# Optimization experiments

Measured on AMD Instinct MI355X. Metric: run time of the kernel, lower is better.

The kernel has to match this reference:

```python
import jax, jax.numpy as jnp
import numpy as np

N_NODES = 20000
N_EDGES = 160000
N_GRAPHS = 64
IN_DIM = 1304  # 1280 + 24
NEG_SLOPE = 0.2


def gat_conv(x, src, dst, W, a_src, a_dst, b, heads, out_ch):
    """PyG-style GATConv (source_to_target flow, self loops already appended).
    x: [N, in], W: [in, heads*out], a_src/a_dst: [heads, out], b: [heads*out].
    Returns [N, heads*out] (concat=True)."""
    N = x.shape[0]
    h = (x @ W).reshape(N, heads, out_ch)                 # [N, H, C]
    e_src = jnp.sum(h * a_src[None], axis=-1)             # [N, H]
    e_dst = jnp.sum(h * a_dst[None], axis=-1)             # [N, H]
    e = jax.nn.leaky_relu(e_src[src] + e_dst[dst], NEG_SLOPE)  # [E, H]
    # softmax over incoming edges of each destination node
    e_max = jax.ops.segment_max(e, dst, num_segments=N)   # [N, H]
    e_exp = jnp.exp(e - e_max[dst])
    denom = jax.ops.segment_sum(e_exp, dst, num_segments=N)
    alpha = e_exp / (denom[dst] + 1e-16)                  # [E, H]
    msg = h[src] * alpha[:, :, None]                      # [E, H, C]
    out = jax.ops.segment_sum(msg, dst, num_segments=N)   # [N, H, C]
    return out.reshape(N, heads * out_ch) + b


def setup_inputs() -> dict:
    key = jax.random.key(0)
    ks = jax.random.split(key, 20)
    x = jax.random.normal(ks[0], (N_NODES, IN_DIM), dtype=jnp.float32)
    edge_index = jax.random.randint(ks[1], (2, N_EDGES), 0, N_NODES, dtype=jnp.int32)
    phy = jax.random.normal(ks[2], (N_GRAPHS, 188), dtype=jnp.float32)
    batch = jnp.sort(jax.random.randint(ks[3], (N_NODES,), 0, N_GRAPHS, dtype=jnp.int32))

    def glorot(k, shape):
        fan_in, fan_out = shape[0], shape[-1]
        lim = jnp.sqrt(6.0 / (fan_in + fan_out))
        return jax.random.uniform(k, shape, jnp.float32, -lim, lim)

    params = {
        # conv1: GATConv(1304, 256, heads=3)
        "W1": glorot(ks[4], (IN_DIM, 3 * 256)),
        "a_src1": glorot(ks[5], (3, 256)) * 0.1,
        "a_dst1": glorot(ks[6], (3, 256)) * 0.1,
        "b1": jnp.zeros((3 * 256,), jnp.float32),
        # conv2: GATConv(768, 256, heads=1)
        "W2": glorot(ks[7], (3 * 256, 256)),
        "a_src2": glorot(ks[8], (1, 256)) * 0.1,
        "a_dst2": glorot(ks[9], (1, 256)) * 0.1,
        "b2": jnp.zeros((256,), jnp.float32),
        # fc1
        "fc1_w1": glorot(ks[10], (188, 128)), "fc1_b1": jnp.zeros((128,), jnp.float32),
        "fc1_w2": glorot(ks[11], (128, 128)), "fc1_b2": jnp.zeros((128,), jnp.float32),
        # fc2
        "fc2_w1": glorot(ks[12], (256 + 128, 192)), "fc2_b1": jnp.zeros((192,), jnp.float32),
        "fc2_w2": glorot(ks[13], (192, 2)), "fc2_b2": jnp.zeros((2,), jnp.float32),
    }
    return {"x": x, "edge_index": edge_index, "phy": phy, "batch": batch, **params}


def reference(x, edge_index, phy, batch,
              W1, a_src1, a_dst1, b1,
              W2, a_src2, a_dst2, b2,
              fc1_w1, fc1_b1, fc1_w2, fc1_b2,
              fc2_w1, fc2_b1, fc2_w2, fc2_b2):
    N = x.shape[0]
    # add self loops (PyG GATConv default)
    loops = jnp.arange(N, dtype=edge_index.dtype)
    src = jnp.concatenate([edge_index[0], loops])
    dst = jnp.concatenate([edge_index[1], loops])

    h = gat_conv(x, src, dst, W1, a_src1, a_dst1, b1, heads=3, out_ch=256)
    h = jax.nn.relu(h)  # dropout is identity at inference
    h = gat_conv(h, src, dst, W2, a_src2, a_dst2, b2, heads=1, out_ch=256)

    # global mean pool per graph
    sums = jax.ops.segment_sum(h, batch, num_segments=N_GRAPHS)        # [B, 256]
    cnts = jax.ops.segment_sum(jnp.ones((N,), h.dtype), batch, num_segments=N_GRAPHS)
    pooled = sums / jnp.maximum(cnts, 1.0)[:, None]

    mid = jax.nn.relu(phy @ fc1_w1 + fc1_b1)
    mid = jax.nn.relu(mid @ fc1_w2 + fc1_b2)

    z = jnp.concatenate([pooled, mid], axis=1)                          # [B, 384]
    z = jax.nn.relu(z @ fc2_w1 + fc2_b1)
    logits = z @ fc2_w2 + fc2_b2
    return jax.nn.softmax(logits, axis=1)
```

## Files before the change

### kernel.cpp

```cpp
#include <hip/hip_runtime.h>
#include <hip/hip_bf16.h>
#include <math.h>

#define NN    20000
#define MP1   20224
#define NP    20096
#define E0    160000
#define EL    180000
#define NG    64
#define INDIM 1304
#define K1P   1344
#define GNT   21
#define GNX   3
#define GMB   79
#define NEG_SLOPE 0.2f
#define PCH   8
#define NSB   20

#define ZB    80
#define XB    13272
#define WB    4800

typedef __bf16 bf16x8 __attribute__((ext_vector_type(8)));
typedef __bf16 bf16x4 __attribute__((ext_vector_type(4)));
typedef float  f32x4  __attribute__((ext_vector_type(4)));

__device__ __forceinline__ void gload16(const void* g, void* l) {
    __builtin_amdgcn_global_load_lds(
        (const __attribute__((address_space(1))) void*)g,
        (__attribute__((address_space(3))) void*)l, 16, 0, 0);
}

#define BAR()  { __builtin_amdgcn_s_barrier(); asm volatile("" ::: "memory"); }
#define VMW(n) { asm volatile("s_waitcnt vmcnt(" #n ")" ::: "memory"); __builtin_amdgcn_sched_barrier(0); }

__global__ __launch_bounds__(256)
void init_kernel(uint4* __restrict__ zreg, int n16,
                 const float* __restrict__ X, __hip_bfloat16* __restrict__ Xb,
                 const float* __restrict__ W1, const float* __restrict__ W2,
                 __hip_bfloat16* __restrict__ w1t, __hip_bfloat16* __restrict__ w2t) {
    const int b = blockIdx.x, t = threadIdx.x;
    if (b < ZB) {
        int i = b * 256 + t;
        if (i < n16) zreg[i] = (uint4){0u, 0u, 0u, 0u};
        return;
    }
    if (b < ZB + XB) {
        int idx = (b - ZB) * 256 + t;
        const int nb = K1P / 8;
        int row = idx / nb;
        int cb = (idx - row * nb) * 8;
        union { __hip_bfloat16 h[8]; float4 f4; } u;
        if (row < NN && cb + 8 <= INDIM) {
            const float4* p = (const float4*)(X + (size_t)row * INDIM + cb);
            float4 u0 = p[0], u1 = p[1];
            u.h[0] = __float2bfloat16(u0.x); u.h[1] = __float2bfloat16(u0.y);
            u.h[2] = __float2bfloat16(u0.z); u.h[3] = __float2bfloat16(u0.w);
            u.h[4] = __float2bfloat16(u1.x); u.h[5] = __float2bfloat16(u1.y);
            u.h[6] = __float2bfloat16(u1.z); u.h[7] = __float2bfloat16(u1.w);
        } else {
#pragma unroll
            for (int e = 0; e < 8; e++) {
                float f = (row < NN && cb + e < INDIM) ? X[(size_t)row * INDIM + cb + e] : 0.f;
                u.h[e] = __float2bfloat16(f);
            }
        }
        *(float4*)(Xb + (size_t)row * K1P + cb) = u.f4;
        return;
    }
    {
        int idx = (b - ZB - XB) * 256 + t;
        const int n1 = 768 * K1P;
        if (idx < n1) {
            int n = idx / K1P, k = idx - n * K1P;
            float f = (k < INDIM) ? W1[(size_t)k * 768 + n] : 0.f;
            w1t[idx] = __float2bfloat16(f);
        } else {
            int i2 = idx - n1;
            if (i2 < 256 * 768) {
                int n = i2 / 768, k = i2 - n * 768;
                w2t[i2] = __float2bfloat16(W2[(size_t)k * 256 + n]);
            }
        }
    }
}

__device__ __forceinline__ void stA(const __hip_bfloat16* __restrict__ A, int bm, int kt, int mh,
                                    char* abuf, int w, int l) {
#pragma unroll
    for (int u = 0; u < 2; u++) {
        int rl = (w << 3) + (l >> 3);
        int lrow = u * 128 + mh * 64 + rl;
        int skb = ((l & 7) << 4) ^ ((rl & 7) << 4);
        const char* g = (const char*)(A + (size_t)(bm + lrow) * K1P + kt * 64) + skb;
        gload16(g, abuf + (u * 128 + mh * 64) * 128 + (w << 10));
    }
}

__device__ __forceinline__ void stB(const __hip_bfloat16* __restrict__ Bt, int bn, int kt, int nh,
                                    char* bbuf, int w, int l) {
#pragma unroll
    for (int u = 0; u < 2; u++) {
        int c = u * 2 + (w >> 2);
        int row0 = c * 64 + nh * 32;
        int rl = ((w & 3) << 3) + (l >> 3);
        int skb = ((l & 7) << 4) ^ ((rl & 7) << 4);
        const char* g = (const char*)(Bt + (size_t)(bn + row0 + rl) * K1P + kt * 64) + skb;
        gload16(g, bbuf + row0 * 128 + ((w & 3) << 10));
    }
}

__global__ __launch_bounds__(512)
void gemm256(const __hip_bfloat16* __restrict__ A,
             const __hip_bfloat16* __restrict__ Bt,
             __hip_bfloat16* __restrict__ C,
             const float* __restrict__ a_src, const float* __restrict__ a_dst,
             float* __restrict__ esrc, float* __restrict__ edst, int M) {
    __shared__ char lds[131072];
    const int t = threadIdx.x;
    const int w = t >> 6, l = t & 63;
    const int wm = w >> 2, wn = w & 3;
    const int fr = l & 15, fq = l >> 4;
    const int amask = (fr & 7) << 4;

    const int nwg = GMB * GNX;
    const int q8 = nwg >> 3, r8 = nwg & 7;
    const int xcd = blockIdx.x & 7, sub = blockIdx.x >> 3;
    const int logical = (xcd < r8 ? xcd * (q8 + 1) : r8 * (q8 + 1) + (xcd - r8) * q8) + sub;
    const int bm = (logical / GNX) * 256;
    const int bn = (logical % GNX) * 256;

    f32x4 acc[8][4];
#pragma unroll
    for (int i = 0; i < 8; i++)
#pragma unroll
        for (int j = 0; j < 4; j++) acc[i][j] = (f32x4){0.f, 0.f, 0.f, 0.f};

    char* A0 = lds;            char* B0 = lds + 32768;
    char* A1 = lds + 65536;    char* B1 = lds + 98304;

    stA(A, bm, 0, 0, A0, w, l);
    stB(Bt, bn, 0, 0, B0, w, l);
    stA(A, bm, 0, 1, A0, w, l);
    stB(Bt, bn, 0, 1, B0, w, l);
    stA(A, bm, 1, 0, A1, w, l);
    stB(Bt, bn, 1, 0, B1, w, l);
    VMW(8);
    BAR();

    for (int kt = 0; kt < GNT; kt++) {
        char* Ab = lds + (kt & 1) * 65536;
        char* Bb = Ab + 32768;
        char* An = lds + ((kt + 1) & 1) * 65536;
        char* Bn = An + 32768;
        bf16x8 a_c[4][2], b_c0[2][2], b_c1[2][2];

#pragma unroll
        for (int im = 0; im < 4; im++)
#pragma unroll
            for (int kk = 0; kk < 2; kk++)
                a_c[im][kk] = *(const bf16x8*)(Ab + (wm * 128 + im * 16 + fr) * 128 + ((kk * 64 + fq * 16) ^ amask));
#pragma unroll
        for (int jn = 0; jn < 2; jn++)
#pragma unroll
            for (int kk = 0; kk < 2; kk++)
                b_c0[jn][kk] = *(const bf16x8*)(Bb + (wn * 64 + jn * 16 + fr) * 128 + ((kk * 64 + fq * 16) ^ amask));
        if (kt + 1 < GNT) stA(A, bm, kt + 1, 1, An, w, l);
        BAR();
        __builtin_amdgcn_s_setprio(1);
#pragma unroll
        for (int im = 0; im < 4; im++)
#pragma unroll
            for (int jn = 0; jn < 2; jn++)
#pragma unroll
                for (int kk = 0; kk < 2; kk++)
                    acc[im][jn] = __builtin_amdgcn_mfma_f32_16x16x32_bf16(a_c[im][kk], b_c0[jn][kk], acc[im][jn], 0, 0, 0);
        __builtin_amdgcn_s_setprio(0);
        if (kt == GNT - 1) { VMW(0); } else { VMW(6); }
        BAR();

#pragma unroll
        for (int jn = 0; jn < 2; jn++)
#pragma unroll
            for (int kk = 0; kk < 2; kk++)
                b_c1[jn][kk] = *(const bf16x8*)(Bb + (wn * 64 + 32 + jn * 16 + fr) * 128 + ((kk * 64 + fq * 16) ^ amask));
        if (kt + 1 < GNT) stB(Bt, bn, kt + 1, 1, Bn, w, l);
        BAR();
        __builtin_amdgcn_s_setprio(1);
#pragma unroll
        for (int im = 0; im < 4; im++)
#pragma unroll
            for (int jn = 0; jn < 2; jn++)
#pragma unroll
                for (int kk = 0; kk < 2; kk++)
                    acc[im][2 + jn] = __builtin_amdgcn_mfma_f32_16x16x32_bf16(a_c[im][kk], b_c1[jn][kk], acc[im][2 + jn], 0, 0, 0);
        __builtin_amdgcn_s_setprio(0);
        if (kt == GNT - 1) { VMW(2); } else { VMW(10); }
        BAR();

#pragma unroll
        for (int im = 0; im < 4; im++)
#pragma unroll
            for (int kk = 0; kk < 2; kk++)
                a_c[im][kk] = *(const bf16x8*)(Ab + (wm * 128 + 64 + im * 16 + fr) * 128 + ((kk * 64 + fq * 16) ^ amask));
        if (kt + 2 < GNT) stA(A, bm, kt + 2, 0, Ab, w, l);
        BAR();
        __builtin_amdgcn_s_setprio(1);
#pragma unroll
        for (int im = 0; im < 4; im++)
#pragma unroll
            for (int jn = 0; jn < 2; jn++)
#pragma unroll
                for (int kk = 0; kk < 2; kk++)
                    acc[4 + im][jn] = __builtin_amdgcn_mfma_f32_16x16x32_bf16(a_c[im][kk], b_c0[jn][kk], acc[4 + im][jn], 0, 0, 0);
        __builtin_amdgcn_s_setprio(0);
        BAR();

        if (kt + 2 < GNT) stB(Bt, bn, kt + 2, 0, Bb, w, l);
        BAR();
        __builtin_amdgcn_s_setprio(1);
#pragma unroll
        for (int im = 0; im < 4; im++)
#pragma unroll
            for (int jn = 0; jn < 2; jn++)
#pragma unroll
                for (int kk = 0; kk < 2; kk++)
                    acc[4 + im][2 + jn] = __builtin_amdgcn_mfma_f32_16x16x32_bf16(a_c[im][kk], b_c1[jn][kk], acc[4 + im][2 + jn], 0, 0, 0);
        __builtin_amdgcn_s_setprio(0);
        if (kt + 2 < GNT) { VMW(8); }
        else if (kt + 2 == GNT) { VMW(4); }
        BAR();
    }

#pragma unroll
    for (int i = 0; i < 8; i++)
#pragma unroll
        for (int j = 0; j < 4; j++)
#pragma unroll
            for (int r = 0; r < 4; r++) {
                int row = bm + wm * 128 + i * 16 + fq * 4 + r;
                int col = bn + wn * 64 + j * 16 + fr;
                if (row < M) C[(size_t)row * 768 + col] = __float2bfloat16(acc[i][j][r]);
            }

    const int head = bn >> 8;
    float asv[4], adv[4];
#pragma unroll
    for (int j = 0; j < 4; j++) {
        asv[j] = a_src[head * 256 + wn * 64 + j * 16 + fr];
        adv[j] = a_dst[head * 256 + wn * 64 + j * 16 + fr];
    }
    __syncthreads();
    float* eb = (float*)lds;
#pragma unroll
    for (int i = 0; i < 8; i++) {
#pragma unroll
        for (int r = 0; r < 4; r++) {
            float ps = 0.f, pd = 0.f;
#pragma unroll
            for (int j = 0; j < 4; j++) { ps += acc[i][j][r] * asv[j]; pd += acc[i][j][r] * adv[j]; }
#pragma unroll
            for (int o = 8; o >= 1; o >>= 1) { ps += __shfl_xor(ps, o, 64); pd += __shfl_xor(pd, o, 64); }
            if (fr == 0) {
                int rowl = wm * 128 + i * 16 + fq * 4 + r;
                eb[(rowl * 4 + wn) * 2 + 0] = ps;
                eb[(rowl * 4 + wn) * 2 + 1] = pd;
            }
        }
    }
    __syncthreads();
    if (t < 256) {
        int row = bm + t;
        if (row < M) {
            float s = eb[t * 8 + 0] + eb[t * 8 + 2] + eb[t * 8 + 4] + eb[t * 8 + 6];
            float d = eb[t * 8 + 1] + eb[t * 8 + 3] + eb[t * 8 + 5] + eb[t * 8 + 7];
            esrc[row * 3 + head] = s;
            edst[row * 3 + head] = d;
        }
    }
}

__global__ __launch_bounds__(256)
void gemm2_fused(const __hip_bfloat16* __restrict__ A,
                 const __hip_bfloat16* __restrict__ Bt,
                 __hip_bfloat16* __restrict__ C,
                 const float* __restrict__ a_src2, const float* __restrict__ a_dst2,
                 float* __restrict__ esrc, float* __restrict__ edst,
                 int M, int N, int K, int NX) {
    __shared__ __hip_bfloat16 As[2][128 * 32];
    __shared__ __hip_bfloat16 Bs[2][128 * 32];
    const int t = threadIdx.x;
    const int w = t >> 6;
    const int l = t & 63;

    const int nwg = gridDim.x;
    const int q = nwg >> 3, r = nwg & 7;
    const int xcd = blockIdx.x & 7, idx = blockIdx.x >> 3;
    const int logical = (xcd < r ? xcd * (q + 1) : r * (q + 1) + (xcd - r) * q) + idx;
    const int bm = (logical / NX) * 128;
    const int bn = (logical % NX) * 128;

    const int wm = (w >> 1) * 64;
    const int wn = (w & 1) * 64;

    f32x4 acc[4][4];
#pragma unroll
    for (int i = 0; i < 4; i++)
#pragma unroll
        for (int j = 0; j < 4; j++) acc[i][j] = (f32x4){0.f, 0.f, 0.f, 0.f};

    const int sr = t >> 2;
    const int sc = (t & 3) * 8;
    const __hip_bfloat16* a0 = A  + (size_t)(bm + sr)      * K + sc;
    const __hip_bfloat16* a1 = A  + (size_t)(bm + 64 + sr) * K + sc;
    const __hip_bfloat16* b0 = Bt + (size_t)(bn + sr)      * K + sc;
    const __hip_bfloat16* b1 = Bt + (size_t)(bn + 64 + sr) * K + sc;

    const int fr = l & 15;
    const int fq = l >> 4;
    const int NT = K / 32;

    auto stage = [&](int k0, int b) {
        char* asb = (char*)&As[b][0];
        char* bsb = (char*)&Bs[b][0];
        gload16(a0 + k0, asb + w * 1024);
        gload16(a1 + k0, asb + 4096 + w * 1024);
        gload16(b0 + k0, bsb + w * 1024);
        gload16(b1 + k0, bsb + 4096 + w * 1024);
    };

    stage(0, 0);
    __syncthreads();

    for (int kt = 0; kt < NT; kt++) {
        const int cb = kt & 1;
        if (kt + 1 < NT) stage((kt + 1) * 32, cb ^ 1);
        bf16x8 av[4], bv[4];
#pragma unroll
        for (int i = 0; i < 4; i++)
            av[i] = *(const bf16x8*)&As[cb][(wm + i * 16 + fr) * 32 + fq * 8];
#pragma unroll
        for (int j = 0; j < 4; j++)
            bv[j] = *(const bf16x8*)&Bs[cb][(wn + j * 16 + fr) * 32 + fq * 8];
#pragma unroll
        for (int i = 0; i < 4; i++)
#pragma unroll
            for (int j = 0; j < 4; j++)
                acc[i][j] = __builtin_amdgcn_mfma_f32_16x16x32_bf16(av[i], bv[j], acc[i][j], 0, 0, 0);
        __syncthreads();
    }

#pragma unroll
    for (int i = 0; i < 4; i++) {
#pragma unroll
        for (int j = 0; j < 4; j++) {
#pragma unroll
            for (int r2 = 0; r2 < 4; r2++) {
                int row = bm + wm + i * 16 + fq * 4 + r2;
                int col = bn + wn + j * 16 + fr;
                if (row < M) C[(size_t)row * N + col] = __float2bfloat16(acc[i][j][r2]);
            }
        }
    }

    float asv[4], adv[4];
#pragma unroll
    for (int j = 0; j < 4; j++) {
        asv[j] = a_src2[bn + wn + j * 16 + fr];
        adv[j] = a_dst2[bn + wn + j * 16 + fr];
    }
    __syncthreads();
    float* eb = (float*)&As[0][0];
#pragma unroll
    for (int i = 0; i < 4; i++) {
#pragma unroll
        for (int r2 = 0; r2 < 4; r2++) {
            float ps = 0.f, pd = 0.f;
#pragma unroll
            for (int j = 0; j < 4; j++) { ps += acc[i][j][r2] * asv[j]; pd += acc[i][j][r2] * adv[j]; }
#pragma unroll
            for (int o = 8; o >= 1; o >>= 1) { ps += __shfl_xor(ps, o, 64); pd += __shfl_xor(pd, o, 64); }
            if (fr == 0) {
                int rowl = wm + i * 16 + fq * 4 + r2;
                int wnIdx = wn >> 6;
                eb[(rowl * 2 + wnIdx) * 2 + 0] = ps;
                eb[(rowl * 2 + wnIdx) * 2 + 1] = pd;
            }
        }
    }
    __syncthreads();
    if (t < 128) {
        int row = bm + t;
        if (row < M) {
            atomicAdd(&esrc[row], eb[t * 4 + 0] + eb[t * 4 + 2]);
            atomicAdd(&edst[row], eb[t * 4 + 1] + eb[t * 4 + 3]);
        }
    }
}

__global__ void hist_kernel(const int* __restrict__ ei, int* __restrict__ deg) {
    int e = blockIdx.x * 256 + threadIdx.x;
    if (e >= EL) return;
    int d = (e < E0) ? ei[E0 + e] : (e - E0);
    atomicAdd(&deg[d], 1);
}

__global__ __launch_bounds__(1024)
void scan_blk(const int* __restrict__ deg, int* __restrict__ off, int* __restrict__ bsum) {
    __shared__ int wsum[16];
    const int b = blockIdx.x, t = threadIdx.x, lane = t & 63, wv = t >> 6;
    const int i = b * 1024 + t;
    int v = (i < NN) ? deg[i] : 0;
    int x = v;
#pragma unroll
    for (int o = 1; o < 64; o <<= 1) {
        int y = __shfl_up(x, o, 64);
        if (lane >= o) x += y;
    }
    if (lane == 63) wsum[wv] = x;
    __syncthreads();
    if (wv == 0 && lane < 16) {
        int s = wsum[lane];
#pragma unroll
        for (int o = 1; o < 16; o <<= 1) {
            int y = __shfl_up(s, o, 64);
            if (lane >= o) s += y;
        }
        wsum[lane] = s;
    }
    __syncthreads();
    int woff = (wv == 0) ? 0 : wsum[wv - 1];
    if (i < NN) off[i + 1] = woff + x;
    if (t == 1023) bsum[b] = wsum[15];
}

__global__ __launch_bounds__(1024)
void scan_add(int* __restrict__ off, const int* __restrict__ bsum) {
    __shared__ int boffs[NSB];
    const int b = blockIdx.x, t = threadIdx.x;
    if (t < 64) {
        int lane = t;
        int v = (lane < NSB) ? bsum[lane] : 0;
        int x = v;
#pragma unroll
        for (int o = 1; o < 64; o <<= 1) {
            int y = __shfl_up(x, o, 64);
            if (lane >= o) x += y;
        }
        if (lane < NSB) boffs[lane] = x - v;
    }
    __syncthreads();
    const int i = b * 1024 + t;
    if (i < NN) off[i + 1] += boffs[b];
    if (b == 0 && t == 0) off[0] = 0;
}

__global__ void fill_kernel(const int* __restrict__ ei, const int* __restrict__ off,
                            int* __restrict__ cur, int* __restrict__ csr) {
    int e = blockIdx.x * 256 + threadIdx.x;
    if (e >= EL) return;
    int d = (e < E0) ? ei[E0 + e] : (e - E0);
    int s = (e < E0) ? ei[e] : (e - E0);
    int pos = off[d] + atomicAdd(&cur[d], 1);
    csr[pos] = s;
}

template<int H, bool RELU, typename OutT>
__global__ __launch_bounds__(256)
void gat_aggregate(const __hip_bfloat16* __restrict__ hfeat,
                   const float* __restrict__ esrc,
                   const float* __restrict__ edst,
                   const int* __restrict__ off, const int* __restrict__ csr,
                   const float* __restrict__ bias,
                   OutT* __restrict__ out, int N) {
    const int wv = threadIdx.x >> 6, lane = threadIdx.x & 63;
    const int n = blockIdx.x * 4 + wv;
    if (n >= N) return;
    const int beg = off[n];
    const int deg = off[n + 1] - beg;

    float ed[H], m[H], den[H];
    f32x4 acc[H];
#pragma unroll
    for (int h = 0; h < H; h++) {
        ed[h] = edst[n * H + h];
        m[h] = -INFINITY;
        den[h] = 0.f;
        acc[h] = (f32x4){0.f, 0.f, 0.f, 0.f};
    }

    for (int base = 0; base < deg; base += 64) {
        const int i = base + lane;
        int s = 0;
        float lg[H];
        if (i < deg) {
            s = csr[beg + i];
#pragma unroll
            for (int h = 0; h < H; h++) {
                float v = esrc[s * H + h] + ed[h];
                lg[h] = (v >= 0.f) ? v : NEG_SLOPE * v;
            }
        } else {
#pragma unroll
            for (int h = 0; h < H; h++) lg[h] = -INFINITY;
        }
        float cm[H];
#pragma unroll
        for (int h = 0; h < H; h++) {
            cm[h] = lg[h];
#pragma unroll
            for (int o = 1; o < 64; o <<= 1)
                cm[h] = fmaxf(cm[h], __shfl_xor(cm[h], o, 64));
        }
#pragma unroll
        for (int h = 0; h < H; h++) {
            float nm = fmaxf(m[h], cm[h]);
            float sc = expf(m[h] - nm);
            den[h] *= sc;
#pragma unroll
            for (int e = 0; e < 4; e++) acc[h][e] *= sc;
            m[h] = nm;
        }
        float wgt[H];
#pragma unroll
        for (int h = 0; h < H; h++) {
            wgt[h] = (i < deg) ? expf(lg[h] - m[h]) : 0.f;
            den[h] += wgt[h];
        }
        const int cnt = min(64, deg - base);
        for (int j = 0; j < cnt; j++) {
            int sj = __shfl(s, j, 64);
#pragma unroll
            for (int h = 0; h < H; h++) {
                float wj = __shfl(wgt[h], j, 64);
                bf16x4 hv = *(const bf16x4*)(hfeat + (size_t)sj * (H * 256) + h * 256 + 4 * lane);
#pragma unroll
                for (int e = 0; e < 4; e++) acc[h][e] += wj * (float)hv[e];
            }
        }
    }
#pragma unroll
    for (int h = 0; h < H; h++) {
#pragma unroll
        for (int o = 1; o < 64; o <<= 1) den[h] += __shfl_xor(den[h], o, 64);
    }
#pragma unroll
    for (int h = 0; h < H; h++) {
        float inv = 1.f / (den[h] + 1e-16f);
        if constexpr (sizeof(OutT) == 2) {
            bf16x4 r;
#pragma unroll
            for (int e = 0; e < 4; e++) {
                float f = acc[h][e] * inv + bias[h * 256 + 4 * lane + e];
                if (RELU) f = fmaxf(f, 0.f);
                r[e] = (__bf16)f;
            }
            *(bf16x4*)((__hip_bfloat16*)out + (size_t)n * (H * 256) + h * 256 + 4 * lane) = r;
        } else {
            float4 r;
            float* rp = &r.x;
#pragma unroll
            for (int e = 0; e < 4; e++) {
                float f = acc[h][e] * inv + bias[h * 256 + 4 * lane + e];
                if (RELU) f = fmaxf(f, 0.f);
                rp[e] = f;
            }
            *(float4*)((float*)out + (size_t)n * (H * 256) + h * 256 + 4 * lane) = r;
        }
    }
}

__device__ __forceinline__ int lower_bound_batch(const int* __restrict__ batch, int key) {
    int lo = 0, hi = NN;
    while (lo < hi) {
        int mid = (lo + hi) >> 1;
        if (batch[mid] < key) lo = mid + 1; else hi = mid;
    }
    return lo;
}

__global__ __launch_bounds__(256)
void pool_partial(const __hip_bfloat16* __restrict__ out2, const int* __restrict__ batch,
                  float* __restrict__ partial, float* __restrict__ cnts) {
    const int g = blockIdx.x, c = blockIdx.y, t = threadIdx.x;
    const int s = lower_bound_batch(batch, g);
    const int e = lower_bound_batch(batch, g + 1);
    float acc = 0.f;
    for (int n = s + c; n < e; n += PCH) acc += __bfloat162float(out2[(size_t)n * 256 + t]);
    partial[((size_t)g * PCH + c) * 256 + t] = acc;
    if (t == 0 && c == 0) cnts[g] = (float)(e - s);
}

__global__ __launch_bounds__(256)
void head_kernel(const float* __restrict__ phy, const float* __restrict__ partial,
                 const float* __restrict__ cnts,
                 const float* __restrict__ w11, const float* __restrict__ b11,
                 const float* __restrict__ w12, const float* __restrict__ b12,
                 const float* __restrict__ w21, const float* __restrict__ b21,
                 const float* __restrict__ w22, const float* __restrict__ b22,
                 float* __restrict__ out) {
    int g = blockIdx.x, t = threadIdx.x;
    __shared__ float ph[188];
    __shared__ float z[384];
    __shared__ float mid[128];
    __shared__ float t1[192];
    __shared__ float lg[2];
    if (t < 188) ph[t] = phy[g * 188 + t];
    {
        float s = 0.f;
#pragma unroll
        for (int c = 0; c < PCH; c++) s += partial[((size_t)g * PCH + c) * 256 + t];
        z[t] = s / fmaxf(cnts[g], 1.0f);
    }
    __syncthreads();
    if (t < 128) {
        float s = b11[t];
        for (int k = 0; k < 188; k++) s += ph[k] * w11[k * 128 + t];
        mid[t] = fmaxf(s, 0.f);
    }
    __syncthreads();
    if (t < 128) {
        float s = b12[t];
        for (int k = 0; k < 128; k++) s += mid[k] * w12[k * 128 + t];
        z[256 + t] = fmaxf(s, 0.f);
    }
    __syncthreads();
    if (t < 192) {
        float s = b21[t];
        for (int k = 0; k < 384; k++) s += z[k] * w21[k * 192 + t];
        t1[t] = fmaxf(s, 0.f);
    }
    __syncthreads();
    if (t < 2) {
        float s = b22[t];
        for (int k = 0; k < 192; k++) s += t1[k] * w22[k * 2 + t];
        lg[t] = s;
    }
    __syncthreads();
    if (t == 0) {
        float mx = fmaxf(lg[0], lg[1]);
        float e0 = expf(lg[0] - mx), e1 = expf(lg[1] - mx);
        float d = e0 + e1;
        out[g * 2 + 0] = e0 / d;
        out[g * 2 + 1] = e1 / d;
    }
}

extern "C" void kernel_launch(void* const* d_in, const int* in_sizes, int n_in,
                              void* d_out, int out_size, void* d_ws, size_t ws_size,
                              hipStream_t stream) {
    const float* x       = (const float*)d_in[0];
    const int*   ei      = (const int*)  d_in[1];
    const float* phy     = (const float*)d_in[2];
    const int*   batch   = (const int*)  d_in[3];
    const float* W1      = (const float*)d_in[4];
    const float* a_src1  = (const float*)d_in[5];
    const float* a_dst1  = (const float*)d_in[6];
    const float* b1      = (const float*)d_in[7];
    const float* W2      = (const float*)d_in[8];
    const float* a_src2  = (const float*)d_in[9];
    const float* a_dst2  = (const float*)d_in[10];
    const float* b2      = (const float*)d_in[11];
    const float* fc1_w1  = (const float*)d_in[12];
    const float* fc1_b1  = (const float*)d_in[13];
    const float* fc1_w2  = (const float*)d_in[14];
    const float* fc1_b2  = (const float*)d_in[15];
    const float* fc2_w1  = (const float*)d_in[16];
    const float* fc2_b1  = (const float*)d_in[17];
    const float* fc2_w2  = (const float*)d_in[18];
    const float* fc2_b2  = (const float*)d_in[19];
    float* out = (float*)d_out;

    char* base = (char*)d_ws;
    size_t o = 0;
    auto alloc = [&](size_t bytes) { size_t r = o; o += (bytes + 255) & ~255ULL; return r; };

    size_t o_xb   = alloc((size_t)MP1 * K1P * 2);
    size_t o_w1t  = alloc((size_t)768 * K1P * 2);
    size_t o_w2t  = alloc((size_t)256 * 768 * 2);
    size_t o_h1b  = alloc((size_t)NP * 768 * 2);
    size_t o_hob  = alloc((size_t)NP * 768 * 2);
    size_t o_es1  = alloc((size_t)NN * 3 * 4);
    size_t o_ed1  = alloc((size_t)NN * 3 * 4);
    size_t o_es2  = alloc((size_t)NN * 4);
    size_t o_ed2  = alloc((size_t)NN * 4);
    size_t o_deg  = alloc((size_t)(NN + 1) * 4);
    size_t o_cur  = alloc((size_t)NN * 4);
    size_t o_zend = o;
    size_t o_off  = alloc((size_t)(NN + 1) * 4);
    size_t o_csr  = alloc((size_t)EL * 4);
    size_t o_bsum = alloc((size_t)NSB * 4);
    size_t o_part = alloc((size_t)NG * PCH * 256 * 4);
    size_t o_cnts = alloc((size_t)NG * 4);
    (void)o_cnts;

    __hip_bfloat16* xb   = (__hip_bfloat16*)(base + o_xb);
    __hip_bfloat16* w1t  = (__hip_bfloat16*)(base + o_w1t);
    __hip_bfloat16* w2t  = (__hip_bfloat16*)(base + o_w2t);
    __hip_bfloat16* h1b  = (__hip_bfloat16*)(base + o_h1b);
    __hip_bfloat16* hob  = (__hip_bfloat16*)(base + o_hob);
    __hip_bfloat16* h2b  = (__hip_bfloat16*)(base + o_xb);
    __hip_bfloat16* out2 = (__hip_bfloat16*)(base + o_xb + (size_t)24 * 1024 * 1024);
    float* es1   = (float*)(base + o_es1);
    float* ed1   = (float*)(base + o_ed1);
    float* es2   = (float*)(base + o_es2);
    float* ed2   = (float*)(base + o_ed2);
    int*   deg   = (int*)(base + o_deg);
    int*   cur   = (int*)(base + o_cur);
    int*   offs  = (int*)(base + o_off);
    int*   csr   = (int*)(base + o_csr);
    int*   bsum  = (int*)(base + o_bsum);
    float* part  = (float*)(base + o_part);
    float* cnts  = (float*)(base + o_cnts);

    {
        int n16 = (int)((o_zend - o_es2) / 16);
        init_kernel<<<ZB + XB + WB, 256, 0, stream>>>((uint4*)(base + o_es2), n16,
                                                      x, xb, W1, W2, w1t, w2t);
    }

    hist_kernel<<<(EL + 255) / 256, 256, 0, stream>>>(ei, deg);
    scan_blk<<<NSB, 1024, 0, stream>>>(deg, offs, bsum);
    scan_add<<<NSB, 1024, 0, stream>>>(offs, bsum);
    fill_kernel<<<(EL + 255) / 256, 256, 0, stream>>>(ei, offs, cur, csr);

    gemm256<<<GMB * GNX, 512, 0, stream>>>(xb, w1t, h1b, a_src1, a_dst1, es1, ed1, NN);
    gat_aggregate<3, true, __hip_bfloat16><<<(NN + 3) / 4, 256, 0, stream>>>(h1b, es1, ed1, offs, csr, b1, hob, NN);

    gemm2_fused<<<2 * 157, 256, 0, stream>>>(hob, w2t, h2b, a_src2, a_dst2, es2, ed2, NN, 256, 768, 2);
    gat_aggregate<1, false, __hip_bfloat16><<<(NN + 3) / 4, 256, 0, stream>>>(h2b, es2, ed2, offs, csr, b2, out2, NN);

    pool_partial<<<dim3(NG, PCH), 256, 0, stream>>>(out2, batch, part, cnts);
    head_kernel<<<NG, 256, 0, stream>>>(phy, part, cnts,
                                        fc1_w1, fc1_b1, fc1_w2, fc1_b2,
                                        fc2_w1, fc2_b1, fc2_w2, fc2_b2, out);
}
```

Measured before the change: 243.5 us.

## Fuse CSR fill into GEMM1 launch and pooling into head kernel

The CSR fill step now runs as extra workgroups appended to the first GEMM launch, so it overlaps with the GEMM instead of taking its own launch. Global mean pooling moves into the head kernel: 512 threads per graph sum the rows in two stripes, which removes the pool_partial launch and its partial buffer. This cuts two kernel launches. In exchange, pooling in the head kernel has much less parallelism (64 blocks in place of 512), and the fill blocks have to share the GPU with the GEMM workgroups, each of which reserves 128KB of LDS.

New measurement: 260.5 us. +7.0%, slower.

```diff
diff --git a/kernel.cpp b/kernel.cpp
--- a/kernel.cpp
+++ b/kernel.cpp
@@ -13,8 +13,9 @@
 #define GNT   21
 #define GNX   3
 #define GMB   79
+#define NWG1  (GMB * GNX)
+#define FB    ((EL + 511) / 512)
 #define NEG_SLOPE 0.2f
-#define PCH   8
 #define NSB   20
 
 #define ZB    80
@@ -115,15 +116,29 @@
              const __hip_bfloat16* __restrict__ Bt,
              __hip_bfloat16* __restrict__ C,
              const float* __restrict__ a_src, const float* __restrict__ a_dst,
-             float* __restrict__ esrc, float* __restrict__ edst, int M) {
+             float* __restrict__ esrc, float* __restrict__ edst, int M,
+             const int* __restrict__ ei, const int* __restrict__ off,
+             int* __restrict__ cur, int* __restrict__ csr) {
     __shared__ char lds[131072];
     const int t = threadIdx.x;
+
+    if (blockIdx.x >= NWG1) {
+        int e = (blockIdx.x - NWG1) * 512 + t;
+        if (e < EL) {
+            int d = (e < E0) ? ei[E0 + e] : (e - E0);
+            int s = (e < E0) ? ei[e] : (e - E0);
+            int pos = off[d] + atomicAdd(&cur[d], 1);
+            csr[pos] = s;
+        }
+        return;
+    }
+
     const int w = t >> 6, l = t & 63;
     const int wm = w >> 2, wn = w & 3;
     const int fr = l & 15, fq = l >> 4;
     const int amask = (fr & 7) << 4;
 
-    const int nwg = GMB * GNX;
+    const int nwg = NWG1;
     const int q8 = nwg >> 3, r8 = nwg & 7;
     const int xcd = blockIdx.x & 7, sub = blockIdx.x >> 3;
     const int logical = (xcd < r8 ? xcd * (q8 + 1) : r8 * (q8 + 1) + (xcd - r8) * q8) + sub;
@@ -453,16 +468,6 @@
     const int i = b * 1024 + t;
     if (i < NN) off[i + 1] += boffs[b];
     if (b == 0 && t == 0) off[0] = 0;
-}
-
-__global__ void fill_kernel(const int* __restrict__ ei, const int* __restrict__ off,
-                            int* __restrict__ cur, int* __restrict__ csr) {
-    int e = blockIdx.x * 256 + threadIdx.x;
-    if (e >= EL) return;
-    int d = (e < E0) ? ei[E0 + e] : (e - E0);
-    int s = (e < E0) ? ei[e] : (e - E0);
-    int pos = off[d] + atomicAdd(&cur[d], 1);
-    csr[pos] = s;
 }
 
 template<int H, bool RELU, typename OutT>
@@ -579,62 +584,60 @@
     return lo;
 }
 
-__global__ __launch_bounds__(256)
-void pool_partial(const __hip_bfloat16* __restrict__ out2, const int* __restrict__ batch,
-                  float* __restrict__ partial, float* __restrict__ cnts) {
-    const int g = blockIdx.x, c = blockIdx.y, t = threadIdx.x;
-    const int s = lower_bound_batch(batch, g);
-    const int e = lower_bound_batch(batch, g + 1);
-    float acc = 0.f;
-    for (int n = s + c; n < e; n += PCH) acc += __bfloat162float(out2[(size_t)n * 256 + t]);
-    partial[((size_t)g * PCH + c) * 256 + t] = acc;
-    if (t == 0 && c == 0) cnts[g] = (float)(e - s);
-}
-
-__global__ __launch_bounds__(256)
-void head_kernel(const float* __restrict__ phy, const float* __restrict__ partial,
-                 const float* __restrict__ cnts,
+__global__ __launch_bounds__(512)
+void head_kernel(const __hip_bfloat16* __restrict__ out2, const int* __restrict__ batch,
+                 const float* __restrict__ phy,
                  const float* __restrict__ w11, const float* __restrict__ b11,
                  const float* __restrict__ w12, const float* __restrict__ b12,
                  const float* __restrict__ w21, const float* __restrict__ b21,
                  const float* __restrict__ w22, const float* __restrict__ b22,
                  float* __restrict__ out) {
     int g = blockIdx.x, t = threadIdx.x;
+    __shared__ float pbuf[512];
     __shared__ float ph[188];
     __shared__ float z[384];
     __shared__ float mid[128];
     __shared__ float t1[192];
     __shared__ float lg[2];
+
+    const int s = lower_bound_batch(batch, g);
+    const int e = lower_bound_batch(batch, g + 1);
+    {
+        const int col = t & 255, stripe = t >> 8;
+        float acc = 0.f;
+        for (int n = s + stripe; n < e; n += 2)
+            acc += __bfloat162float(out2[(size_t)n * 256 + col]);
+        pbuf[t] = acc;
+    }
     if (t < 188) ph[t] = phy[g * 188 + t];
-    {
-        float s = 0.f;
-#pragma unroll
-        for (int c = 0; c < PCH; c++) s += partial[((size_t)g * PCH + c) * 256 + t];
-        z[t] = s / fmaxf(cnts[g], 1.0f);
+    __syncthreads();
+    if (t < 256) {
+        float cnt = fmaxf((float)(e - s), 1.0f);
+        z[t] = (pbuf[t] + pbuf[t + 256]) / cnt;
     }
     __syncthreads();
     if (t < 128) {
-        float s = b11[t];
-        for (int k = 0; k < 188; k++) s += ph[k] * w11[k * 128 + t];
-        mid[t] = fmaxf(s, 0.f);
+        float sm = b11[t];
+        for (int k = 0; k < 188; k++) sm += ph[k] * w11[k * 128 + t];
+        mid[t] = fmaxf(sm, 0.f);
     }
     __syncthreads();
     if (t < 128) {
-        float s = b12[t];
-        for (int k = 0; k < 128; k++) s += mid[k] * w12[k * 128 + t];
-        z[256 + t] = fmaxf(s, 0.f);
+        float sm = b12[t];
+        for (int k = 0; k < 128; k++) sm += mid[k] * w12[k * 128 + t];
+        z[256 + t] = fmaxf(sm, 0.f);
     }
     __syncthreads();
     if (t < 192) {
-        float s = b21[t];
-        for (int k = 0; k < 384; k++) s += z[k] * w21[k * 192 + t];
-        t1[t] = fmaxf(s, 0.f);
+        float sm = b21[t];
+        for (int k = 0; k < 384; k++) sm += z[k] * w21[k * 192 + t];
+        t1[t] = fmaxf(sm, 0.f);
     }
     __syncthreads();
     if (t < 2) {
-        float s = b22[t];
-        for (int k = 0; k < 192; k++) s += t1[k] * w22[k * 2 + t];
-        lg[t] = s;
+        float sm = b22[t];
+        for (int k = 0; k < 192; k++) sm += t1[k] * w22[k * 2 + t];
+        lg[t] = sm;
     }
     __syncthreads();
     if (t == 0) {
@@ -690,9 +693,6 @@
     size_t o_off  = alloc((size_t)(NN + 1) * 4);
     size_t o_csr  = alloc((size_t)EL * 4);
     size_t o_bsum = alloc((size_t)NSB * 4);
-    size_t o_part = alloc((size_t)NG * PCH * 256 * 4);
-    size_t o_cnts = alloc((size_t)NG * 4);
-    (void)o_cnts;
 
     __hip_bfloat16* xb   = (__hip_bfloat16*)(base + o_xb);
     __hip_bfloat16* w1t  = (__hip_bfloat16*)(base + o_w1t);
@@ -710,8 +710,6 @@
     int*   offs  = (int*)(base + o_off);
     int*   csr   = (int*)(base + o_csr);
     int*   bsum  = (int*)(base + o_bsum);
-    float* part  = (float*)(base + o_part);
-    float* cnts  = (float*)(base + o_cnts);
 
     {
         int n16 = (int)((o_zend - o_es2) / 16);
@@ -722,16 +720,15 @@
     hist_kernel<<<(EL + 255) / 256, 256, 0, stream>>>(ei, deg);
     scan_blk<<<NSB, 1024, 0, stream>>>(deg, offs, bsum);
     scan_add<<<NSB, 1024, 0, stream>>>(offs, bsum);
-    fill_kernel<<<(EL + 255) / 256, 256, 0, stream>>>(ei, offs, cur, csr);
-
-    gemm256<<<GMB * GNX, 512, 0, stream>>>(xb, w1t, h1b, a_src1, a_dst1, es1, ed1, NN);
+
+    gemm256<<<NWG1 + FB, 512, 0, stream>>>(xb, w1t, h1b, a_src1, a_dst1, es1, ed1, NN,
+                                           ei, offs, cur, csr);
     gat_aggregate<3, true, __hip_bfloat16><<<(NN + 3) / 4, 256, 0, stream>>>(h1b, es1, ed1, offs, csr, b1, hob, NN);
 
     gemm2_fused<<<2 * 157, 256, 0, stream>>>(hob, w2t, h2b, a_src2, a_dst2, es2, ed2, NN, 256, 768, 2);
     gat_aggregate<1, false, __hip_bfloat16><<<(NN + 3) / 4, 256, 0, stream>>>(h2b, es2, ed2, offs, csr, b2, out2, NN);
 
-    pool_partial<<<dim3(NG, PCH), 256, 0, stream>>>(out2, batch, part, cnts);
-    head_kernel<<<NG, 256, 0, stream>>>(phy, part, cnts,
+    head_kernel<<<NG, 512, 0, stream>>>(out2, batch, phy,
                                         fc1_w1, fc1_b1, fc1_w2, fc1_b2,
                                         fc2_w1, fc2_b1, fc2_w2, fc2_b2, out);
 }
```
